# Optimization experiments

Measured on AMD Instinct MI355X. Metric: run time of the kernel, lower is better.

The kernel has to match this reference:

```python
import jax, jax.numpy as jnp
import numpy as np

B, L, E, DK = 16, 2048, 1024, 128
MODE = "Decoder"


def setup_inputs() -> dict:
    key = jax.random.key(0)
    ks = jax.random.split(key, 6)
    x = jax.random.normal(ks[0], (B, L, E), dtype=jnp.float32)
    context = jax.random.normal(ks[1], (B, L, E), dtype=jnp.float32)
    batch_lengths = jax.random.randint(ks[2], (B,), 1, L + 1)  # valid lengths in [1, L]
    Wq = jax.random.normal(ks[3], (E, DK), dtype=jnp.float32) * 0.02
    Wk = jax.random.normal(ks[4], (E, DK), dtype=jnp.float32) * 0.02
    Wv = jax.random.normal(ks[5], (E, DK), dtype=jnp.float32) * 0.02
    return {"x": x, "context": context, "batch_lengths": batch_lengths,
            "Wq": Wq, "Wk": Wk, "Wv": Wv, "max_len": L}


def reference(x, context, batch_lengths, Wq, Wk, Wv, max_len):
    # x, context: [B, L, E]; batch_lengths: [B] ints; weights: [E, DK]
    Lq = x.shape[1]
    dk = Wq.shape[1]
    pos = jnp.arange(Lq)
    # outputMask: zero out padded time steps, broadcast over feature dim [B, L, 1]
    len_mask = (pos[None, :] < batch_lengths[:, None]).astype(x.dtype)[:, :, None]
    Q = (context @ Wq) * len_mask
    K = (context @ Wk) * len_mask
    V = (x @ Wv) * len_mask
    # energy: [B, Lq, Lk]
    energy = jnp.einsum("bqd,bkd->bqk", Q, K)
    # attnMask: -inf on padded key positions
    key_valid = pos[None, None, :] < batch_lengths[:, None, None]  # [B,1,Lk]
    if MODE == "Decoder":
        causal = pos[None, :, None] >= pos[None, None, :]  # j <= i
        key_valid = key_valid & causal
    energy = jnp.where(key_valid, energy, -jnp.inf)
    score = jax.nn.softmax(energy / jnp.sqrt(jnp.asarray(dk, x.dtype)), axis=-1)
    return jnp.einsum("bqk,bkd->bqd", score, V)
```

## Files before the change

kernel.cpp:

```cpp
#include <hip/hip_runtime.h>

#define DEV __device__ __forceinline__

typedef __attribute__((ext_vector_type(4))) float f32x4;
typedef __attribute__((ext_vector_type(4))) unsigned short u16x4;
typedef __attribute__((ext_vector_type(8))) __bf16 bf16x8;

constexpr int NB = 16, SL = 2048, EM = 1024, DKD = 128;

DEV unsigned short f2bf(float f) {
  unsigned int u = __float_as_uint(f);
  u += 0x7FFFu + ((u >> 16) & 1u);
  return (unsigned short)(u >> 16);
}

DEV f32x4 mfma16(bf16x8 a, bf16x8 b, f32x4 c) {
  return __builtin_amdgcn_mfma_f32_16x16x32_bf16(a, b, c, 0, 0, 0);
}

DEV void dma16(const void* g, void* l) {
  __builtin_amdgcn_global_load_lds(
      (const __attribute__((address_space(1))) unsigned int*)g,
      (__attribute__((address_space(3))) unsigned int*)l, 16, 0, 0);
}

DEV bf16x8 cvt8(f32x4 a, f32x4 b) {
  bf16x8 r;
  r[0] = (__bf16)a[0]; r[1] = (__bf16)a[1]; r[2] = (__bf16)a[2]; r[3] = (__bf16)a[3];
  r[4] = (__bf16)b[0]; r[5] = (__bf16)b[1]; r[6] = (__bf16)b[2]; r[7] = (__bf16)b[3];
  return r;
}

#define SBAR() __builtin_amdgcn_sched_barrier(0)

__global__ __launch_bounds__(256) void prep_w(
    const float* __restrict__ Wq, const float* __restrict__ Wk,
    const float* __restrict__ Wv, unsigned short* __restrict__ Wt,
    float* __restrict__ mvg)
{
  __shared__ unsigned short T[64 * 128];
  const int tid = threadIdx.x;
  if (blockIdx.x == 0) {
    #pragma unroll
    for (int i = 0; i < NB * DKD / 256; ++i) mvg[i * 256 + tid] = 0.f;
  }
  const int m = blockIdx.x >> 4, kc = blockIdx.x & 15;
  const float* W = (m == 0) ? Wq : ((m == 1) ? Wk : Wv);
  #pragma unroll
  for (int it = 0; it < 8; ++it) {
    int idx = it * 256 + tid;
    int kk = idx >> 5, n4 = (idx & 31) * 4;
    f32x4 w4 = *(const f32x4*)(W + (size_t)(kc * 64 + kk) * DKD + n4);
    *(u16x4*)&T[kk * 128 + n4] =
        u16x4{ f2bf(w4[0]), f2bf(w4[1]), f2bf(w4[2]), f2bf(w4[3]) };
  }
  __syncthreads();
  #pragma unroll
  for (int it = 0; it < 4; ++it) {
    int idx = it * 256 + tid;
    int p = idx & 7, n = idx >> 3;
    int c = p ^ (n & 7);
    unsigned short v[8];
    #pragma unroll
    for (int e = 0; e < 8; ++e) v[e] = T[(c * 8 + e) * 128 + n];
    size_t t = ((size_t)(m * 16 + kc) * 128 + n) * 8 + p;
    *(u16x4*)(Wt + t * 8)     = u16x4{v[0], v[1], v[2], v[3]};
    *(u16x4*)(Wt + t * 8 + 4) = u16x4{v[4], v[5], v[6], v[7]};
  }
}

__global__ __launch_bounds__(256, 2) void proj_qk(
    const float* __restrict__ ctx, const unsigned short* __restrict__ Wt,
    const int* __restrict__ lens, unsigned short* __restrict__ Qo,
    unsigned short* __restrict__ Kz)
{
  __shared__ float Als[4][64 * 64];
  const int tid = threadIdx.x;
  const int wave = tid >> 6, lane = tid & 63;
  const int quad = lane >> 4, mm = lane & 15;
  const int rb = blockIdx.x * 64;
  const int len = lens[blockIdx.x >> 5];
  if ((rb & (SL - 1)) >= len) return;

  f32x4 acc[4][4];
  #pragma unroll
  for (int i = 0; i < 4; ++i)
    #pragma unroll
    for (int j = 0; j < 4; ++j) acc[i][j] = f32x4{0.f, 0.f, 0.f, 0.f};

  const float* asrc[4];
  #pragma unroll
  for (int i = 0; i < 4; ++i) {
    const int rl_ = wave * 16 + i * 4 + (lane >> 4);
    const int cc  = (lane & 8) | ((lane & 7) ^ (rl_ & 7));
    asrc[i] = ctx + (size_t)(rb + rl_) * EM + cc * 4;
  }
  int soff[2][2];
  #pragma unroll
  for (int ks = 0; ks < 2; ++ks) {
    soff[ks][0] = (ks * 8 + ((quad * 2)     ^ (mm & 7))) * 4;
    soff[ks][1] = (ks * 8 + ((quad * 2 + 1) ^ (mm & 7))) * 4;
  }
  const unsigned short* bbase[4][2];
  #pragma unroll
  for (int lo = 0; lo < 4; ++lo)
    #pragma unroll
    for (int ks = 0; ks < 2; ++ks) {
      const int nrow = (wave * 4 + lo) * 16 + mm;
      const int pp = (ks * 4 + quad) ^ (mm & 7);
      const int cs = nrow * 8 + pp;
      bbase[lo][ks] = Wt + ((size_t)(cs >> 10) * 16384 + (cs & 1023)) * 8;
    }

  #pragma unroll
  for (int i = 0; i < 4; ++i) dma16(asrc[i],       (char*)Als[0] + wave * 4096 + i * 1024);
  #pragma unroll
  for (int i = 0; i < 4; ++i) dma16(asrc[i] + 64,  (char*)Als[1] + wave * 4096 + i * 1024);
  SBAR();
  bf16x8 bA[4][2], bB[4][2];
  #pragma unroll
  for (int lo = 0; lo < 4; ++lo)
    #pragma unroll
    for (int ks = 0; ks < 2; ++ks) {
      bA[lo][ks] = *(const bf16x8*)(bbase[lo][ks]);
      bB[lo][ks] = *(const bf16x8*)(bbase[lo][ks] + 8192);
    }
  SBAR();
  #pragma unroll
  for (int i = 0; i < 4; ++i) dma16(asrc[i] + 128, (char*)Als[2] + wave * 4096 + i * 1024);
  #pragma unroll
  for (int i = 0; i < 4; ++i) dma16(asrc[i] + 192, (char*)Als[3] + wave * 4096 + i * 1024);
  SBAR();
  __asm__ volatile("s_waitcnt vmcnt(24)" ::: "memory");
  __builtin_amdgcn_s_barrier();
  SBAR();

  #pragma unroll 1
  for (int s = 0; s < 8; ++s) {
    const int kc0 = 2 * s, kc1 = 2 * s + 1;
    bf16x8 af0[4][2];
    #pragma unroll
    for (int rt = 0; rt < 4; ++rt) {
      const float* rbase = Als[kc0 & 3] + (rt * 16 + mm) * 64;
      #pragma unroll
      for (int ks = 0; ks < 2; ++ks)
        af0[rt][ks] = cvt8(*(const f32x4*)(rbase + soff[ks][0]),
                           *(const f32x4*)(rbase + soff[ks][1]));
    }
    #pragma unroll
    for (int lo = 0; lo < 4; ++lo)
      #pragma unroll
      for (int ks = 0; ks < 2; ++ks)
        #pragma unroll
        for (int rt = 0; rt < 4; ++rt)
          acc[rt][lo] = mfma16(af0[rt][ks], bA[lo][ks], acc[rt][lo]);
    {
      const int kn = (kc0 + 2 < 16) ? (kc0 + 2) : 15;
      #pragma unroll
      for (int lo = 0; lo < 4; ++lo)
        #pragma unroll
        for (int ks = 0; ks < 2; ++ks)
          bA[lo][ks] = *(const bf16x8*)(bbase[lo][ks] + (size_t)kn * 8192);
    }
    bf16x8 af1[4][2];
    #pragma unroll
    for (int rt = 0; rt < 4; ++rt) {
      const float* rbase = Als[kc1 & 3] + (rt * 16 + mm) * 64;
      #pragma unroll
      for (int ks = 0; ks < 2; ++ks)
        af1[rt][ks] = cvt8(*(const f32x4*)(rbase + soff[ks][0]),
                           *(const f32x4*)(rbase + soff[ks][1]));
    }
    #pragma unroll
    for (int lo = 0; lo < 4; ++lo)
      #pragma unroll
      for (int ks = 0; ks < 2; ++ks)
        #pragma unroll
        for (int rt = 0; rt < 4; ++rt)
          acc[rt][lo] = mfma16(af1[rt][ks], bB[lo][ks], acc[rt][lo]);
    {
      const int kn = (kc0 + 3 < 16) ? (kc0 + 3) : 15;
      #pragma unroll
      for (int lo = 0; lo < 4; ++lo)
        #pragma unroll
        for (int ks = 0; ks < 2; ++ks)
          bB[lo][ks] = *(const bf16x8*)(bbase[lo][ks] + (size_t)kn * 8192);
    }
    __asm__ volatile("s_waitcnt lgkmcnt(0)" ::: "memory");
    SBAR();
    __builtin_amdgcn_s_barrier();
    {
      const int k4 = (kc0 + 4 < 16) ? (kc0 + 4) : 15;
      const int k5 = (kc0 + 5 < 16) ? (kc0 + 5) : 15;
      #pragma unroll
      for (int i = 0; i < 4; ++i)
        dma16(asrc[i] + k4 * 64, (char*)Als[kc0 & 3] + wave * 4096 + i * 1024);
      #pragma unroll
      for (int i = 0; i < 4; ++i)
        dma16(asrc[i] + k5 * 64, (char*)Als[kc1 & 3] + wave * 4096 + i * 1024);
    }
    __asm__ volatile("s_waitcnt vmcnt(24)" ::: "memory");
    __builtin_amdgcn_s_barrier();
    SBAR();
  }
  __asm__ volatile("s_waitcnt vmcnt(0)" ::: "memory");

  const float SCALE = 1.4426950408889634f * 0.08838834764831845f;
  #pragma unroll
  for (int rt = 0; rt < 4; ++rt)
    #pragma unroll
    for (int lo = 0; lo < 4; ++lo) {
      const int ctg = wave * 4 + lo;
      #pragma unroll
      for (int reg = 0; reg < 4; ++reg) {
        const int row = rb + rt * 16 + quad * 4 + reg;
        const int j = row & (SL - 1);
        const float val = acc[rt][lo][reg];
        if (ctg < 8) {
          const int d = ctg * 16 + mm;
          Qo[(size_t)row * DKD + d] = f2bf(val * ((j < len) ? SCALE : 0.f));
        } else {
          const int d = (ctg - 8) * 16 + mm;
          Kz[(size_t)row * DKD + (((d >> 3) ^ (j & 15)) * 8) + (d & 7)] = f2bf(val);
        }
      }
    }
}

__global__ __launch_bounds__(256, 2) void proj_v(
    const float* __restrict__ x, const unsigned short* __restrict__ Wt,
    const int* __restrict__ lens, unsigned short* __restrict__ Vz,
    float* __restrict__ mvg)
{
  __shared__ float Als[4][64 * 64];
  const int tid = threadIdx.x;
  const int wave = tid >> 6, lane = tid & 63;
  const int quad = lane >> 4, mm = lane & 15;
  const int rb = blockIdx.x * 64;
  const int bidx = blockIdx.x >> 5;
  const int len = lens[bidx];
  if ((rb & (SL - 1)) >= len) return;

  f32x4 acc[4][2];
  #pragma unroll
  for (int i = 0; i < 4; ++i) { acc[i][0] = f32x4{0.f,0.f,0.f,0.f}; acc[i][1] = f32x4{0.f,0.f,0.f,0.f}; }

  const float* asrc[4];
  #pragma unroll
  for (int i = 0; i < 4; ++i) {
    const int rl_ = wave * 16 + i * 4 + (lane >> 4);
    const int cc  = (lane & 8) | ((lane & 7) ^ (rl_ & 7));
    asrc[i] = x + (size_t)(rb + rl_) * EM + cc * 4;
  }
  int soff[2][2];
  #pragma unroll
  for (int ks = 0; ks < 2; ++ks) {
    soff[ks][0] = (ks * 8 + ((quad * 2)     ^ (mm & 7))) * 4;
    soff[ks][1] = (ks * 8 + ((quad * 2 + 1) ^ (mm & 7))) * 4;
  }
  const unsigned short* bbase[2][2];
  #pragma unroll
  for (int lo = 0; lo < 2; ++lo)
    #pragma unroll
    for (int ks = 0; ks < 2; ++ks) {
      const int nrow = (wave * 2 + lo) * 16 + mm;
      const int pp = (ks * 4 + quad) ^ (mm & 7);
      const int cs = nrow * 8 + pp;
      bbase[lo][ks] = Wt + ((size_t)2 * 16384 + cs) * 8;
    }

  #pragma unroll
  for (int i = 0; i < 4; ++i) dma16(asrc[i],       (char*)Als[0] + wave * 4096 + i * 1024);
  #pragma unroll
  for (int i = 0; i < 4; ++i) dma16(asrc[i] + 64,  (char*)Als[1] + wave * 4096 + i * 1024);
  SBAR();
  bf16x8 bA[2][2], bB[2][2];
  #pragma unroll
  for (int lo = 0; lo < 2; ++lo)
    #pragma unroll
    for (int ks = 0; ks < 2; ++ks) {
      bA[lo][ks] = *(const bf16x8*)(bbase[lo][ks]);
      bB[lo][ks] = *(const bf16x8*)(bbase[lo][ks] + 8192);
    }
  SBAR();
  #pragma unroll
  for (int i = 0; i < 4; ++i) dma16(asrc[i] + 128, (char*)Als[2] + wave * 4096 + i * 1024);
  #pragma unroll
  for (int i = 0; i < 4; ++i) dma16(asrc[i] + 192, (char*)Als[3] + wave * 4096 + i * 1024);
  SBAR();
  __asm__ volatile("s_waitcnt vmcnt(16)" ::: "memory");
  __builtin_amdgcn_s_barrier();
  SBAR();

  #pragma unroll 1
  for (int s = 0; s < 8; ++s) {
    const int kc0 = 2 * s, kc1 = 2 * s + 1;
    bf16x8 af0[4][2];
    #pragma unroll
    for (int rt = 0; rt < 4; ++rt) {
      const float* rbase = Als[kc0 & 3] + (rt * 16 + mm) * 64;
      #pragma unroll
      for (int ks = 0; ks < 2; ++ks)
        af0[rt][ks] = cvt8(*(const f32x4*)(rbase + soff[ks][0]),
                           *(const f32x4*)(rbase + soff[ks][1]));
    }
    #pragma unroll
    for (int lo = 0; lo < 2; ++lo)
      #pragma unroll
      for (int ks = 0; ks < 2; ++ks)
        #pragma unroll
        for (int rt = 0; rt < 4; ++rt)
          acc[rt][lo] = mfma16(af0[rt][ks], bA[lo][ks], acc[rt][lo]);
    {
      const int kn = (kc0 + 2 < 16) ? (kc0 + 2) : 15;
      #pragma unroll
      for (int lo = 0; lo < 2; ++lo)
        #pragma unroll
        for (int ks = 0; ks < 2; ++ks)
          bA[lo][ks] = *(const bf16x8*)(bbase[lo][ks] + (size_t)kn * 8192);
    }
    bf16x8 af1[4][2];
    #pragma unroll
    for (int rt = 0; rt < 4; ++rt) {
      const float* rbase = Als[kc1 & 3] + (rt * 16 + mm) * 64;
      #pragma unroll
      for (int ks = 0; ks < 2; ++ks)
        af1[rt][ks] = cvt8(*(const f32x4*)(rbase + soff[ks][0]),
                           *(const f32x4*)(rbase + soff[ks][1]));
    }
    #pragma unroll
    for (int lo = 0; lo < 2; ++lo)
      #pragma unroll
      for (int ks = 0; ks < 2; ++ks)
        #pragma unroll
        for (int rt = 0; rt < 4; ++rt)
          acc[rt][lo] = mfma16(af1[rt][ks], bB[lo][ks], acc[rt][lo]);
    {
      const int kn = (kc0 + 3 < 16) ? (kc0 + 3) : 15;
      #pragma unroll
      for (int lo = 0; lo < 2; ++lo)
        #pragma unroll
        for (int ks = 0; ks < 2; ++ks)
          bB[lo][ks] = *(const bf16x8*)(bbase[lo][ks] + (size_t)kn * 8192);
    }
    __asm__ volatile("s_waitcnt lgkmcnt(0)" ::: "memory");
    SBAR();
    __builtin_amdgcn_s_barrier();
    {
      const int k4 = (kc0 + 4 < 16) ? (kc0 + 4) : 15;
      const int k5 = (kc0 + 5 < 16) ? (kc0 + 5) : 15;
      #pragma unroll
      for (int i = 0; i < 4; ++i)
        dma16(asrc[i] + k4 * 64, (char*)Als[kc0 & 3] + wave * 4096 + i * 1024);
      #pragma unroll
      for (int i = 0; i < 4; ++i)
        dma16(asrc[i] + k5 * 64, (char*)Als[kc1 & 3] + wave * 4096 + i * 1024);
    }
    __asm__ volatile("s_waitcnt vmcnt(16)" ::: "memory");
    __builtin_amdgcn_s_barrier();
    SBAR();
  }
  __asm__ volatile("s_waitcnt vmcnt(0)" ::: "memory");

  #pragma unroll
  for (int rt = 0; rt < 4; ++rt)
    #pragma unroll
    for (int lo = 0; lo < 2; ++lo) {
      const int d = (wave * 2 + lo) * 16 + mm;
      const int row0 = rb + rt * 16 + quad * 4;
      const int b = row0 >> 11, j0 = row0 & (SL - 1);
      u16x4 pk = u16x4{ f2bf(acc[rt][lo][0]), f2bf(acc[rt][lo][1]),
                        f2bf(acc[rt][lo][2]), f2bf(acc[rt][lo][3]) };
      size_t off = (size_t)b * DKD * SL + (size_t)d * SL + (j0 & ~63)
                 + ((((j0 >> 3) & 7) ^ (d & 7)) * 8) + (j0 & 7);
      *(u16x4*)(Vz + off) = pk;
    }

  const int jb = rb & (SL - 1);
  #pragma unroll
  for (int lo = 0; lo < 2; ++lo) {
    const int d = (wave * 2 + lo) * 16 + mm;
    float part = 0.f;
    #pragma unroll
    for (int rt = 0; rt < 4; ++rt) {
      const int jr = jb + rt * 16 + quad * 4;
      #pragma unroll
      for (int reg = 0; reg < 4; ++reg)
        if (jr + reg < len) part += acc[rt][lo][reg];
    }
    part += __shfl_xor(part, 16);
    part += __shfl_xor(part, 32);
    if (quad == 0) atomicAdd(mvg + bidx * DKD + d, part);
  }
}

__global__ __launch_bounds__(256, 2) void attn(
    const unsigned short* __restrict__ Qw, const unsigned short* __restrict__ Kz,
    const unsigned short* __restrict__ Vz, const float* __restrict__ mvg,
    const int* __restrict__ lens, float* __restrict__ out)
{
  __shared__ unsigned short Ks[2][64 * 128];
  __shared__ unsigned short Vs[2][128 * 64];
  __shared__ unsigned short Ps[4][16 * 72];
  const int tid = threadIdx.x;
  const int wave = tid >> 6, lane = tid & 63;
  const int quad = lane >> 4, mm = lane & 15;
  const int b = blockIdx.y;
  const int qb = ((int)gridDim.x - 1 - (int)blockIdx.x) * 64;
  const int len = lens[b];

  if (qb >= len) {
    const int dd = (tid & 31) * 4;
    const int r0 = tid >> 5;
    const f32x4 m4 = *(const f32x4*)(mvg + b * DKD + dd);
    const float inv = 1.0f / (float)len;
    const f32x4 val = f32x4{ m4[0]*inv, m4[1]*inv, m4[2]*inv, m4[3]*inv };
    #pragma unroll
    for (int it = 0; it < 8; ++it) {
      const int row = qb + it * 8 + r0;
      *(f32x4*)(out + ((size_t)b * SL + row) * DKD + dd) = val;
    }
    return;
  }

  const int kend = min(qb + 64, len);
  const int nblk = (kend + 63) >> 6;
  const int irow0 = qb + wave * 16 + quad * 4;

  bf16x8 aQ[4];
  {
    const unsigned short* qbase =
        Qw + (size_t)(b * SL + qb + wave * 16 + mm) * DKD + quad * 8;
    #pragma unroll
    for (int cc = 0; cc < 4; ++cc) aQ[cc] = *(const bf16x8*)(qbase + cc * 32);
  }
  bf16x8 onesb;
  #pragma unroll
  for (int i = 0; i < 8; ++i) onesb[i] = (__bf16)1.0f;

  float mr[4];
  #pragma unroll
  for (int r = 0; r < 4; ++r) mr[r] = -__builtin_inff();
  f32x4 acc[8];
  #pragma unroll
  for (int i = 0; i < 8; ++i) acc[i] = f32x4{0.f,0.f,0.f,0.f};
  f32x4 accl = f32x4{0.f,0.f,0.f,0.f};

  #pragma unroll
  for (int it = 0; it < 4; ++it) {
    int s = it * 256 + tid;
    dma16(Kz + (size_t)(b * SL) * DKD + (size_t)s * 8,
          (char*)Ks[0] + (it * 256 + wave * 64) * 16);
  }
  #pragma unroll
  for (int it = 0; it < 4; ++it) {
    int s = it * 256 + tid;
    int d = s >> 3, p = s & 7;
    dma16(Vz + (size_t)b * DKD * SL + (size_t)d * SL + p * 8,
          (char*)Vs[0] + (it * 256 + wave * 64) * 16);
  }

  #pragma unroll 1
  for (int blk = 0; blk < nblk; ++blk) {
    const int kb = blk * 64;
    __syncthreads();
    if (blk + 1 < nblk) {
      const int kb1 = kb + 64;
      const int nb = (blk + 1) & 1;
      #pragma unroll
      for (int it = 0; it < 4; ++it) {
        int s = it * 256 + tid;
        dma16(Kz + (size_t)(b * SL + kb1) * DKD + (size_t)s * 8,
              (char*)Ks[nb] + (it * 256 + wave * 64) * 16);
      }
      #pragma unroll
      for (int it = 0; it < 4; ++it) {
        int s = it * 256 + tid;
        int d = s >> 3, p = s & 7;
        dma16(Vz + (size_t)b * DKD * SL + (size_t)d * SL + kb1 + p * 8,
              (char*)Vs[nb] + (it * 256 + wave * 64) * 16);
      }
    }
    const unsigned short* kbuf = Ks[blk & 1];
    const unsigned short* vbuf = Vs[blk & 1];

    f32x4 s4[4];
    __builtin_amdgcn_s_setprio(1);
    #pragma unroll
    for (int nt = 0; nt < 4; ++nt) {
      f32x4 c = f32x4{0.f,0.f,0.f,0.f};
      const int j = nt * 16 + mm;
      #pragma unroll
      for (int cc = 0; cc < 4; ++cc) {
        const int pp = (cc * 4 + quad) ^ mm;
        bf16x8 kf = *(const bf16x8*)(kbuf + j * 128 + pp * 8);
        c = mfma16(aQ[cc], kf, c);
      }
      s4[nt] = c;
    }
    __builtin_amdgcn_s_setprio(0);

    float alpha[4];
    #pragma unroll
    for (int reg = 0; reg < 4; ++reg) {
      const int jl = min(irow0 + reg + 1, len);
      float v0 = (kb + mm      < jl) ? s4[0][reg] : -__builtin_inff();
      float v1 = (kb + 16 + mm < jl) ? s4[1][reg] : -__builtin_inff();
      float v2 = (kb + 32 + mm < jl) ? s4[2][reg] : -__builtin_inff();
      float v3 = (kb + 48 + mm < jl) ? s4[3][reg] : -__builtin_inff();
      float mx = fmaxf(fmaxf(v0, v1), fmaxf(v2, v3));
      #pragma unroll
      for (int xm = 1; xm < 16; xm <<= 1) mx = fmaxf(mx, __shfl_xor(mx, xm));
      const float mn = fmaxf(mr[reg], mx);
      alpha[reg] = __builtin_amdgcn_exp2f(mr[reg] - mn);
      const float p0 = __builtin_amdgcn_exp2f(v0 - mn);
      const float p1 = __builtin_amdgcn_exp2f(v1 - mn);
      const float p2 = __builtin_amdgcn_exp2f(v2 - mn);
      const float p3 = __builtin_amdgcn_exp2f(v3 - mn);
      mr[reg] = mn;
      const int prow = quad * 4 + reg;
      Ps[wave][prow * 72 + mm]      = f2bf(p0);
      Ps[wave][prow * 72 + 16 + mm] = f2bf(p1);
      Ps[wave][prow * 72 + 32 + mm] = f2bf(p2);
      Ps[wave][prow * 72 + 48 + mm] = f2bf(p3);
    }
    #pragma unroll
    for (int nt = 0; nt < 8; ++nt) {
      f32x4 a = acc[nt];
      a[0] *= alpha[0]; a[1] *= alpha[1]; a[2] *= alpha[2]; a[3] *= alpha[3];
      acc[nt] = a;
    }
    accl[0] *= alpha[0]; accl[1] *= alpha[1];
    accl[2] *= alpha[2]; accl[3] *= alpha[3];
    __asm__ volatile("s_waitcnt lgkmcnt(0)" ::: "memory");
    bf16x8 aP[2];
    #pragma unroll
    for (int ks = 0; ks < 2; ++ks)
      aP[ks] = *(const bf16x8*)(&Ps[wave][mm * 72 + ks * 32 + quad * 8]);
    __builtin_amdgcn_s_setprio(1);
    #pragma unroll
    for (int ks = 0; ks < 2; ++ks) {
      #pragma unroll
      for (int nt = 0; nt < 8; ++nt) {
        const int pp = (ks * 4 + quad) ^ (mm & 7);
        bf16x8 vf = *(const bf16x8*)(vbuf + (nt * 16 + mm) * 64 + pp * 8);
        acc[nt] = mfma16(aP[ks], vf, acc[nt]);
      }
      accl = mfma16(aP[ks], onesb, accl);
    }
    __builtin_amdgcn_s_setprio(0);
  }

  #pragma unroll
  for (int reg = 0; reg < 4; ++reg) {
    const float rl = 1.0f / accl[reg];
    const size_t base = ((size_t)b * SL + irow0 + reg) * DKD + mm;
    #pragma unroll
    for (int nt = 0; nt < 8; ++nt)
      out[base + nt * 16] = acc[nt][reg] * rl;
  }
}

extern "C" void kernel_launch(void* const* d_in, const int* in_sizes, int n_in,
                              void* d_out, int out_size, void* d_ws, size_t ws_size,
                              hipStream_t stream) {
  const float* x    = (const float*)d_in[0];
  const float* ctx  = (const float*)d_in[1];
  const int*   lens = (const int*)d_in[2];
  const float* Wq   = (const float*)d_in[3];
  const float* Wk   = (const float*)d_in[4];
  const float* Wv   = (const float*)d_in[5];
  float* out = (float*)d_out;

  const size_t QKV = (size_t)NB * SL * DKD * sizeof(unsigned short);
  const size_t WTSZ = (size_t)3 * 16 * 128 * 8 * 8 * sizeof(unsigned short);
  const size_t MVSZ = (size_t)NB * DKD * sizeof(float);
  if (ws_size < 3 * QKV + WTSZ + MVSZ) return;
  unsigned short* Qws = (unsigned short*)d_ws;
  unsigned short* Kzs = (unsigned short*)((char*)d_ws + QKV);
  unsigned short* Vzs = (unsigned short*)((char*)d_ws + 2 * QKV);
  unsigned short* Wt  = (unsigned short*)((char*)d_ws + 3 * QKV);
  float*          mvg = (float*)((char*)d_ws + 3 * QKV + WTSZ);

  prep_w <<<dim3(48), 256, 0, stream>>>(Wq, Wk, Wv, Wt, mvg);
  proj_qk<<<dim3(NB * SL / 64), 256, 0, stream>>>(ctx, Wt, lens, Qws, Kzs);
  proj_v <<<dim3(NB * SL / 64), 256, 0, stream>>>(x, Wt, lens, Vzs, mvg);
  attn   <<<dim3(SL / 64, NB), 256, 0, stream>>>(Qws, Kzs, Vzs, mvg, lens, out);
}
```

Before: 348.4 us.

## Split each attention key block across two wave groups and merge partial softmax

The attention kernel moves to 512 threads per block. Two groups of four waves each take one 64-key half of a 128-key tile, keeping separate running max, sum and accumulators. The partial results are merged through LDS at the end with a log-sum-exp rescale, which halves the serial key-loop length per block and adds parallelism along the key dimension. In exchange, LDS use roughly doubles to about 146KB, likely limiting the CU to one block. The change also adds an extra merge phase with two barriers and clamps the running max so fully masked halves do not produce NaNs.

Result: faster. 333.4 us (-4.3%).

```diff
diff --git a/kernel.cpp b/kernel.cpp
--- a/kernel.cpp
+++ b/kernel.cpp
@@ -394,17 +394,19 @@
   }
 }
 
-__global__ __launch_bounds__(256, 2) void attn(
+__global__ __launch_bounds__(512, 2) void attn(
     const unsigned short* __restrict__ Qw, const unsigned short* __restrict__ Kz,
     const unsigned short* __restrict__ Vz, const float* __restrict__ mvg,
     const int* __restrict__ lens, float* __restrict__ out)
 {
-  __shared__ unsigned short Ks[2][64 * 128];
-  __shared__ unsigned short Vs[2][128 * 64];
-  __shared__ unsigned short Ps[4][16 * 72];
+  __shared__ unsigned short Ks[2][128 * 128];
+  __shared__ unsigned short Vs[2][2][128 * 64];
+  __shared__ unsigned short Ps[8][16 * 72];
   const int tid = threadIdx.x;
   const int wave = tid >> 6, lane = tid & 63;
   const int quad = lane >> 4, mm = lane & 15;
+  const int wg = wave & 3;
+  const int wh = wave >> 2;
   const int b = blockIdx.y;
   const int qb = ((int)gridDim.x - 1 - (int)blockIdx.x) * 64;
   const int len = lens[b];
@@ -416,21 +418,21 @@
     const float inv = 1.0f / (float)len;
     const f32x4 val = f32x4{ m4[0]*inv, m4[1]*inv, m4[2]*inv, m4[3]*inv };
     #pragma unroll
-    for (int it = 0; it < 8; ++it) {
-      const int row = qb + it * 8 + r0;
+    for (int it = 0; it < 4; ++it) {
+      const int row = qb + it * 16 + r0;
       *(f32x4*)(out + ((size_t)b * SL + row) * DKD + dd) = val;
     }
     return;
   }
 
   const int kend = min(qb + 64, len);
-  const int nblk = (kend + 63) >> 6;
-  const int irow0 = qb + wave * 16 + quad * 4;
+  const int nblk = (kend + 127) >> 7;
+  const int irow0 = qb + wg * 16 + quad * 4;
 
   bf16x8 aQ[4];
   {
     const unsigned short* qbase =
-        Qw + (size_t)(b * SL + qb + wave * 16 + mm) * DKD + quad * 8;
+        Qw + (size_t)(b * SL + qb + wg * 16 + mm) * DKD + quad * 8;
     #pragma unroll
     for (int cc = 0; cc < 4; ++cc) aQ[cc] = *(const bf16x8*)(qbase + cc * 32);
   }
@@ -448,48 +450,53 @@
 
   #pragma unroll
   for (int it = 0; it < 4; ++it) {
-    int s = it * 256 + tid;
+    int s = it * 512 + tid;
     dma16(Kz + (size_t)(b * SL) * DKD + (size_t)s * 8,
-          (char*)Ks[0] + (it * 256 + wave * 64) * 16);
-  }
-  #pragma unroll
-  for (int it = 0; it < 4; ++it) {
-    int s = it * 256 + tid;
-    int d = s >> 3, p = s & 7;
-    dma16(Vz + (size_t)b * DKD * SL + (size_t)d * SL + p * 8,
-          (char*)Vs[0] + (it * 256 + wave * 64) * 16);
-  }
+          (char*)Ks[0] + (it * 512 + wave * 64) * 16);
+  }
+  #pragma unroll
+  for (int h = 0; h < 2; ++h)
+    #pragma unroll
+    for (int it = 0; it < 2; ++it) {
+      int s = it * 512 + tid;
+      int d = s >> 3, p = s & 7;
+      dma16(Vz + (size_t)b * DKD * SL + (size_t)d * SL + h * 64 + p * 8,
+            (char*)Vs[0][h] + (it * 512 + wave * 64) * 16);
+    }
 
   #pragma unroll 1
   for (int blk = 0; blk < nblk; ++blk) {
-    const int kb = blk * 64;
+    const int kb = blk * 128;
     __syncthreads();
     if (blk + 1 < nblk) {
-      const int kb1 = kb + 64;
+      const int kb1 = kb + 128;
       const int nb = (blk + 1) & 1;
       #pragma unroll
       for (int it = 0; it < 4; ++it) {
-        int s = it * 256 + tid;
+        int s = it * 512 + tid;
         dma16(Kz + (size_t)(b * SL + kb1) * DKD + (size_t)s * 8,
-              (char*)Ks[nb] + (it * 256 + wave * 64) * 16);
+              (char*)Ks[nb] + (it * 512 + wave * 64) * 16);
       }
       #pragma unroll
-      for (int it = 0; it < 4; ++it) {
-        int s = it * 256 + tid;
-        int d = s >> 3, p = s & 7;
-        dma16(Vz + (size_t)b * DKD * SL + (size_t)d * SL + kb1 + p * 8,
-              (char*)Vs[nb] + (it * 256 + wave * 64) * 16);
-      }
+      for (int h = 0; h < 2; ++h)
+        #pragma unroll
+        for (int it = 0; it < 2; ++it) {
+          int s = it * 512 + tid;
+          int d = s >> 3, p = s & 7;
+          dma16(Vz + (size_t)b * DKD * SL + (size_t)d * SL + (kb1 + h * 64) + p * 8,
+                (char*)Vs[nb][h] + (it * 512 + wave * 64) * 16);
+        }
     }
     const unsigned short* kbuf = Ks[blk & 1];
-    const unsigned short* vbuf = Vs[blk & 1];
+    const unsigned short* vbuf = Vs[blk & 1][wh];
+    const int kbh = kb + wh * 64;
 
     f32x4 s4[4];
     __builtin_amdgcn_s_setprio(1);
     #pragma unroll
     for (int nt = 0; nt < 4; ++nt) {
       f32x4 c = f32x4{0.f,0.f,0.f,0.f};
-      const int j = nt * 16 + mm;
+      const int j = wh * 64 + nt * 16 + mm;
       #pragma unroll
       for (int cc = 0; cc < 4; ++cc) {
         const int pp = (cc * 4 + quad) ^ mm;
@@ -504,14 +511,14 @@
     #pragma unroll
     for (int reg = 0; reg < 4; ++reg) {
       const int jl = min(irow0 + reg + 1, len);
-      float v0 = (kb + mm      < jl) ? s4[0][reg] : -__builtin_inff();
-      float v1 = (kb + 16 + mm < jl) ? s4[1][reg] : -__builtin_inff();
-      float v2 = (kb + 32 + mm < jl) ? s4[2][reg] : -__builtin_inff();
-      float v3 = (kb + 48 + mm < jl) ? s4[3][reg] : -__builtin_inff();
+      float v0 = (kbh + mm      < jl) ? s4[0][reg] : -__builtin_inff();
+      float v1 = (kbh + 16 + mm < jl) ? s4[1][reg] : -__builtin_inff();
+      float v2 = (kbh + 32 + mm < jl) ? s4[2][reg] : -__builtin_inff();
+      float v3 = (kbh + 48 + mm < jl) ? s4[3][reg] : -__builtin_inff();
       float mx = fmaxf(fmaxf(v0, v1), fmaxf(v2, v3));
       #pragma unroll
       for (int xm = 1; xm < 16; xm <<= 1) mx = fmaxf(mx, __shfl_xor(mx, xm));
-      const float mn = fmaxf(mr[reg], mx);
+      const float mn = fmaxf(fmaxf(mr[reg], mx), -1e30f);
       alpha[reg] = __builtin_amdgcn_exp2f(mr[reg] - mn);
       const float p0 = __builtin_amdgcn_exp2f(v0 - mn);
       const float p1 = __builtin_amdgcn_exp2f(v1 - mn);
@@ -551,13 +558,34 @@
     __builtin_amdgcn_s_setprio(0);
   }
 
-  #pragma unroll
-  for (int reg = 0; reg < 4; ++reg) {
-    const float rl = 1.0f / accl[reg];
-    const size_t base = ((size_t)b * SL + irow0 + reg) * DKD + mm;
+  __syncthreads();
+  float* mrg = (float*)&Ks[0][0];
+  if (wh == 1) {
+    float* p = mrg + (wg * 64 + lane) * 41;
+    #pragma unroll
+    for (int r = 0; r < 4; ++r) p[r] = mr[r];
+    #pragma unroll
+    for (int r = 0; r < 4; ++r) p[4 + r] = accl[r];
     #pragma unroll
     for (int nt = 0; nt < 8; ++nt)
-      out[base + nt * 16] = acc[nt][reg] * rl;
+      #pragma unroll
+      for (int r = 0; r < 4; ++r) p[8 + nt * 4 + r] = acc[nt][r];
+  }
+  __syncthreads();
+  if (wh == 0) {
+    const float* p = mrg + (wg * 64 + lane) * 41;
+    #pragma unroll
+    for (int reg = 0; reg < 4; ++reg) {
+      const float m1 = p[reg], l1 = p[4 + reg];
+      const float m = fmaxf(mr[reg], m1);
+      const float f0 = __builtin_amdgcn_exp2f(mr[reg] - m);
+      const float f1 = __builtin_amdgcn_exp2f(m1 - m);
+      const float rl = 1.0f / (accl[reg] * f0 + l1 * f1);
+      const size_t base = ((size_t)b * SL + irow0 + reg) * DKD + mm;
+      #pragma unroll
+      for (int nt = 0; nt < 8; ++nt)
+        out[base + nt * 16] = (acc[nt][reg] * f0 + p[8 + nt * 4 + reg] * f1) * rl;
+    }
   }
 }
 
@@ -585,5 +613,5 @@
   prep_w <<<dim3(48), 256, 0, stream>>>(Wq, Wk, Wv, Wt, mvg);
   proj_qk<<<dim3(NB * SL / 64), 256, 0, stream>>>(ctx, Wt, lens, Qws, Kzs);
   proj_v <<<dim3(NB * SL / 64), 256, 0, stream>>>(x, Wt, lens, Vzs, mvg);
-  attn   <<<dim3(SL / 64, NB), 256, 0, stream>>>(Qws, Kzs, Vzs, mvg, lens, out);
-}
+  attn   <<<dim3(SL / 64, NB), 512, 0, stream>>>(Qws, Kzs, Vzs, mvg, lens, out);
+}
```
